# Optimization experiments

Hardware: AMD Instinct MI355X
Metric: run time of the kernel (lower is better)

## Reference

```python
import jax, jax.numpy as jnp
import numpy as np
from functools import partial
from jax import lax

THRESHOLD = 1.0
BETA = 4.0

@partial(jax.custom_vjp, nondiff_argnums=(1, 2))
def spike_fn(membrane, threshold, beta):
    # hard threshold forward
    return (membrane >= threshold).astype(membrane.dtype)

def _spike_fwd(membrane, threshold, beta):
    return spike_fn(membrane, threshold, beta), membrane

def _spike_bwd(threshold, beta, membrane, g):
    # fast-sigmoid surrogate gradient: 1 / (1 + beta*|u - theta|)^2
    x = membrane - threshold
    surrogate = 1.0 / (1.0 + beta * jnp.abs(x)) ** 2
    return (g * surrogate,)

spike_fn.defvjp(_spike_fwd, _spike_bwd)


def setup_inputs() -> dict:
    key = jax.random.key(0)
    k1, = jax.random.split(key, 1)
    x = jax.random.normal(k1, (64, 100, 4096), dtype=jnp.float32)
    # log_alpha = log(exp(-1/tau_mem)) = -1/tau_mem, tau_mem = 20.0
    log_alpha = jnp.asarray(-1.0 / 20.0, dtype=jnp.float32)
    return {"x": x, "log_alpha": log_alpha}


def reference(x, log_alpha):
    # x: (batch, time, features)
    alpha = jax.nn.sigmoid(log_alpha)  # membrane decay in (0,1)

    def step(u, xt):
        u = alpha * u + xt                    # leaky integration
        s = spike_fn(u, THRESHOLD, BETA)      # fire
        u = u - s * THRESHOLD                 # subtract-reset
        return u, s

    x_t = jnp.swapaxes(x, 0, 1)               # (T, B, F)
    u0 = jnp.zeros_like(x_t[0])
    _, spikes_t = lax.scan(step, u0, x_t)
    spikes = jnp.swapaxes(spikes_t, 0, 1)      # (B, T, F)
    rate = spikes.mean()
    return spikes, rate
```

## Files before the change

kernel.cpp:

```cpp
#include <hip/hip_runtime.h>
#include <math.h>


constexpr int T_STEPS = 100;
constexpr int F       = 4096;
constexpr int BATCH   = 64;
constexpr int NBLOCKS = BATCH * F / 256;
constexpr long long TOTAL = (long long)BATCH * T_STEPS * F;

__global__ __launch_bounds__(256)
void lif_fwd(const float* __restrict__ x,
             const float* __restrict__ log_alpha,
             float*       __restrict__ out,
             unsigned int* __restrict__ blk_cnt) {
    int idx  = blockIdx.x * 256 + threadIdx.x;
    int b    = idx >> 12;
    int f    = idx & 4095;
    size_t base = (size_t)b * T_STEPS * F + f;

    double la = (double)log_alpha[0];
    float alpha = (float)(1.0 / (1.0 + exp(-la)));

    float u = 0.f;
    unsigned int c = 0;

    #pragma unroll 10
    for (int t = 0; t < T_STEPS; ++t) {
        float xt = x[base + (size_t)t * F];
        u = __fadd_rn(__fmul_rn(alpha, u), xt);
        float s = (u >= 1.0f) ? 1.0f : 0.0f;
        u -= s;
        __builtin_nontemporal_store(s, &out[base + (size_t)t * F]);
        c += (unsigned)s;
    }

    for (int off = 32; off > 0; off >>= 1)
        c += __shfl_down(c, off, 64);

    __shared__ unsigned int wsum[4];
    int lane = threadIdx.x & 63;
    int wid  = threadIdx.x >> 6;
    if (lane == 0) wsum[wid] = c;
    __syncthreads();
    if (threadIdx.x == 0)
        blk_cnt[blockIdx.x] = wsum[0] + wsum[1] + wsum[2] + wsum[3];
}

__global__ __launch_bounds__(256)
void lif_rate(const unsigned int* __restrict__ blk_cnt,
              float* __restrict__ rate_out) {
    unsigned int c = 0;
    #pragma unroll
    for (int i = 0; i < NBLOCKS / 256; ++i)
        c += blk_cnt[threadIdx.x + i * 256];
    for (int off = 32; off > 0; off >>= 1)
        c += __shfl_down(c, off, 64);
    __shared__ unsigned int wsum[4];
    int lane = threadIdx.x & 63;
    int wid  = threadIdx.x >> 6;
    if (lane == 0) wsum[wid] = c;
    __syncthreads();
    if (threadIdx.x == 0) {
        unsigned int s = wsum[0] + wsum[1] + wsum[2] + wsum[3];
        rate_out[0] = (float)((double)s / (double)TOTAL);
    }
}

extern "C" void kernel_launch(void* const* d_in, const int* in_sizes, int n_in,
                              void* d_out, int out_size, void* d_ws, size_t ws_size,
                              hipStream_t stream) {
    const float* x  = (const float*)d_in[0];
    const float* la = (const float*)d_in[1];
    float* out = (float*)d_out;
    unsigned int* blk_cnt = (unsigned int*)d_ws;

    lif_fwd<<<NBLOCKS, 256, 0, stream>>>(x, la, out, blk_cnt);
    lif_rate<<<1, 256, 0, stream>>>(blk_cnt, out + TOTAL);
}
```

Measured before the change: 37.73 us.

## Double-buffer input loads in register chunks and defer spike stores via bitmask

Loads the time series in register chunks of 20 steps with double buffering, so the next chunk's loads are issued while the current chunk's serial recurrence runs. Spikes are packed into a 4-word bitmask and all outputs are stored after the recurrence, and the count comes from popcount. This aims to hide global load latency behind the dependent scan and to separate stores from the compute chain. In exchange it raises register pressure, which can lower occupancy, and it concentrates all stores at the end.

```diff
diff --git a/kernel.cpp b/kernel.cpp
--- a/kernel.cpp
+++ b/kernel.cpp
@@ -3,6 +3,8 @@
 
 
 constexpr int T_STEPS = 100;
+constexpr int CHUNK   = 20;
+constexpr int NCHUNK  = T_STEPS / CHUNK;
 constexpr int F       = 4096;
 constexpr int BATCH   = 64;
 constexpr int NBLOCKS = BATCH * F / 256;
@@ -22,17 +24,41 @@
     float alpha = (float)(1.0 / (1.0 + exp(-la)));
 
     float u = 0.f;
-    unsigned int c = 0;
+    unsigned int mask[4] = {0u, 0u, 0u, 0u};
 
-    #pragma unroll 10
+    float bufA[CHUNK], bufB[CHUNK];
+
+    #pragma unroll
+    for (int j = 0; j < CHUNK; ++j)
+        bufA[j] = x[base + (size_t)j * F];
+
+    #pragma unroll
+    for (int c = 0; c < NCHUNK; ++c) {
+        float* cur = (c & 1) ? bufB : bufA;
+        float* nxt = (c & 1) ? bufA : bufB;
+        if (c + 1 < NCHUNK) {
+            #pragma unroll
+            for (int j = 0; j < CHUNK; ++j)
+                nxt[j] = x[base + (size_t)((c + 1) * CHUNK + j) * F];
+        }
+        #pragma unroll
+        for (int j = 0; j < CHUNK; ++j) {
+            int t = c * CHUNK + j;
+            u = __fadd_rn(__fmul_rn(alpha, u), cur[j]);
+            unsigned int bit = (u >= 1.0f) ? 1u : 0u;
+            mask[t >> 5] |= bit << (t & 31);
+            u -= (u >= 1.0f) ? 1.0f : 0.0f;
+        }
+    }
+
+    #pragma unroll
     for (int t = 0; t < T_STEPS; ++t) {
-        float xt = x[base + (size_t)t * F];
-        u = __fadd_rn(__fmul_rn(alpha, u), xt);
-        float s = (u >= 1.0f) ? 1.0f : 0.0f;
-        u -= s;
+        float s = ((mask[t >> 5] >> (t & 31)) & 1u) ? 1.0f : 0.0f;
         __builtin_nontemporal_store(s, &out[base + (size_t)t * F]);
-        c += (unsigned)s;
     }
+
+    unsigned int c = (unsigned)__popc(mask[0]) + (unsigned)__popc(mask[1])
+                   + (unsigned)__popc(mask[2]) + (unsigned)__popc(mask[3]);
 
     for (int off = 32; off > 0; off >>= 1)
         c += __shfl_down(c, off, 64);
```

Measured after the change: 37.99 us. Within noise of the previous version (+0.7%).
